# Kernel optimization log

Hardware: AMD Instinct MI355X
Metric: run time of the kernel (lower is better)

Reference implementation:

```python
import jax, jax.numpy as jnp
import numpy as np

N = 50000
E = 500000
IN_F = 128
HEADS = 4
NEG_SLOPE = 0.2


def _gatv2_conv(x, src, dst, Wl, Wr, att, bias, concat):
    # PyG GATv2Conv (share_weights=False): x_l = lin_l(x) for source, x_r = lin_r(x) for target
    n = x.shape[0]
    H, C = att.shape
    xl = (x @ Wl.T).reshape(n, H, C)
    xr = (x @ Wr.T).reshape(n, H, C)
    # per-edge: e_ij = att . leaky_relu(xl[j] + xr[i])
    e = jax.nn.leaky_relu(xl[src] + xr[dst], negative_slope=NEG_SLOPE)  # [E,H,C]
    logit = jnp.einsum('ehc,hc->eh', e, att)  # [E,H]
    # segment softmax over destination node
    lmax = jax.ops.segment_max(logit, dst, num_segments=n)
    lmax = jnp.where(jnp.isfinite(lmax), lmax, 0.0)
    w = jnp.exp(logit - lmax[dst])
    denom = jax.ops.segment_sum(w, dst, num_segments=n)
    alpha = w / (denom[dst] + 1e-16)
    # weighted scatter-aggregate of source messages
    out = jax.ops.segment_sum(xl[src] * alpha[:, :, None], dst, num_segments=n)  # [N,H,C]
    if concat:
        return out.reshape(n, H * C) + bias
    return out.mean(axis=1) + bias


def setup_inputs() -> dict:
    key = jax.random.key(0)
    ks = jax.random.split(key, 11)
    s = 0.1
    x = jax.random.normal(ks[0], (N, IN_F), jnp.float32)
    edge_index = jax.random.randint(ks[1], (2, E), 0, N, dtype=jnp.int32)
    # layer 1: in=128 -> heads=4, C=32, concat -> out 128
    Wl1 = jax.random.normal(ks[2], (128, IN_F), jnp.float32) * s
    Wr1 = jax.random.normal(ks[3], (128, IN_F), jnp.float32) * s
    att1 = jax.random.normal(ks[4], (HEADS, 32), jnp.float32) * s
    b1 = jnp.zeros((128,), jnp.float32)
    # layer 2: in=128 -> heads=4, C=64, mean (concat=False) -> out 64
    Wl2 = jax.random.normal(ks[5], (256, 128), jnp.float32) * s
    Wr2 = jax.random.normal(ks[6], (256, 128), jnp.float32) * s
    att2 = jax.random.normal(ks[7], (HEADS, 64), jnp.float32) * s
    b2 = jnp.zeros((64,), jnp.float32)
    return {"x": x, "edge_index": edge_index, "Wl1": Wl1, "Wr1": Wr1, "att1": att1,
            "b1": b1, "Wl2": Wl2, "Wr2": Wr2, "att2": att2, "b2": b2}


def reference(x, edge_index, Wl1, Wr1, att1, b1, Wl2, Wr2, att2, b2):
    n = x.shape[0]
    loops = jnp.arange(n, dtype=edge_index.dtype)
    src = jnp.concatenate([edge_index[0], loops])  # PyG add_self_loops=True
    dst = jnp.concatenate([edge_index[1], loops])
    # dropout inactive (inference); forward body: elu between layers
    h = jax.nn.elu(_gatv2_conv(x, src, dst, Wl1, Wr1, att1, b1, concat=True))
    logits = _gatv2_conv(h, src, dst, Wl2, Wr2, att2, b2, concat=False)
    return logits
```

## Files before the change

### kernel.cpp

```cpp
#include <hip/hip_runtime.h>
#include <hip/hip_bf16.h>
#include <math.h>


typedef _Float16 half2v __attribute__((ext_vector_type(2)));
typedef _Float16 half4v __attribute__((ext_vector_type(4)));
typedef _Float16 half8v __attribute__((ext_vector_type(8)));
typedef float float4v __attribute__((ext_vector_type(4)));

template <int CTRL>
static __device__ __forceinline__ float dppadd(float x) {
  int y = __builtin_amdgcn_update_dpp(0, __float_as_int(x), CTRL, 0xf, 0xf, true);
  return x + __int_as_float(y);
}

static __device__ __forceinline__ float red8dpp(float p) {
  p = dppadd<0xB1>(p);
  p = dppadd<0x4E>(p);
  p = dppadd<0x141>(p);
  return p;
}


__global__ void fused_cvt_count_kernel(
    const float* __restrict__ x,
    const float* __restrict__ wl1, const float* __restrict__ wr1,
    const float* __restrict__ wl2, const float* __restrict__ wr2,
    _Float16* __restrict__ xb, _Float16* __restrict__ wb,
    const int* __restrict__ dst, int* __restrict__ deg, int n4x, int E) {
  int i = blockIdx.x * blockDim.x + threadIdx.x;
  int stride = gridDim.x * blockDim.x;
  int total = n4x + 24576 + E;
  for (; i < total; i += stride) {
    if (i < n4x) {
      float4 v = ((const float4*)x)[i];
      half4v o = {(_Float16)v.x, (_Float16)v.y, (_Float16)v.z, (_Float16)v.w};
      ((half4v*)xb)[i] = o;
    } else if (i < n4x + 24576) {
      int fj = (i - n4x) * 4;
      const float* src;
      int so;
      if (fj < 16384) { src = wl1; so = fj; }
      else if (fj < 32768) { src = wr1; so = fj - 16384; }
      else if (fj < 65536) { src = wl2; so = fj - 32768; }
      else { src = wr2; so = fj - 65536; }
      float4 v = *(const float4*)(src + so);
      half4v o = {(_Float16)v.x, (_Float16)v.y, (_Float16)v.z, (_Float16)v.w};
      *(half4v*)(wb + fj) = o;
    } else {
      atomicAdd(&deg[dst[i - n4x - 24576]], 1);
    }
  }
}


__global__ void partial_kernel(const int* __restrict__ deg, int* __restrict__ partial, int N) {
  int t = threadIdx.x;
  int i = blockIdx.x * 256 + t;
  int v = (i < N) ? deg[i] : 0;
  v += __shfl_xor(v, 1); v += __shfl_xor(v, 2); v += __shfl_xor(v, 4);
  v += __shfl_xor(v, 8); v += __shfl_xor(v, 16); v += __shfl_xor(v, 32);
  __shared__ int ws[4];
  if ((t & 63) == 0) ws[t >> 6] = v;
  __syncthreads();
  if (t == 0) partial[blockIdx.x] = ws[0] + ws[1] + ws[2] + ws[3];
}

__global__ void scan_final_kernel(const int* __restrict__ deg, const int* __restrict__ partial,
                                  int* __restrict__ row_ptr, int* __restrict__ cursor,
                                  int N, int E, int nb) {
  __shared__ int sp[256];
  __shared__ int s[256];
  int t = threadIdx.x;
  int pv = (t < nb) ? partial[t] : 0;
  sp[t] = pv;
  __syncthreads();
  for (int off = 1; off < 256; off <<= 1) {
    int u = (t >= off) ? sp[t - off] : 0;
    __syncthreads();
    sp[t] += u;
    __syncthreads();
  }
  int blockpre = (blockIdx.x > 0) ? sp[blockIdx.x - 1] : 0;
  int i = blockIdx.x * 256 + t;
  int v = (i < N) ? deg[i] : 0;
  s[t] = v;
  __syncthreads();
  for (int off = 1; off < 256; off <<= 1) {
    int u = (t >= off) ? s[t - off] : 0;
    __syncthreads();
    s[t] += u;
    __syncthreads();
  }
  int excl = s[t] - v + blockpre;
  if (i < N) {
    row_ptr[i] = excl;
    cursor[i] = excl;
  }
  if (blockIdx.x == 0 && t == 0) row_ptr[N] = E;
}

__global__ void fill_kernel(const int* __restrict__ src, const int* __restrict__ dst,
                            int* __restrict__ cursor, int* __restrict__ col, int E) {
  int i = blockIdx.x * blockDim.x + threadIdx.x;
  if (i < E) {
    int d = dst[i];
    int pos = atomicAdd(&cursor[d], 1);
    col[pos] = src[i];
  }
}

__global__ __launch_bounds__(256) void gemm_mfma2(
    const _Float16* __restrict__ A, const _Float16* __restrict__ Wa,
    const _Float16* __restrict__ Wb, _Float16* __restrict__ Ca,
    _Float16* __restrict__ Cb, int N, int Oa, int ldC) {
  __shared__ _Float16 lds[32768];
  int t = threadIdx.x;
  int gbase = blockIdx.y * 256;
#pragma unroll
  for (int i = 0; i < 16; ++i) {
    int c = t + i * 256;
    int row = c >> 4, kc = c & 15;
    int grow = gbase + row;
    const _Float16* srcW =
        (grow < Oa) ? (Wa + (size_t)grow * 128) : (Wb + (size_t)(grow - Oa) * 128);
    half8v v = *(const half8v*)(srcW + kc * 8);
    int off16 = (row << 4) | (kc ^ (row & 7));
    *(half8v*)((char*)lds + (off16 << 4)) = v;
  }
  __syncthreads();
  int wv = t >> 6, lane = t & 63;
  int l15 = lane & 15, l4 = lane >> 4;
  int row0 = blockIdx.x * 64 + (wv & 1) * 32;
  int colw = (wv >> 1) * 128;
  int gc = gbase + colw;
  half8v xf[2][4];
#pragma unroll
  for (int rg = 0; rg < 2; ++rg) {
    int r = row0 + rg * 16 + l15;
    bool valid = r < N;
    const half8v* Ar = (const half8v*)(A + (size_t)r * 128 + l4 * 8);
#pragma unroll
    for (int kk = 0; kk < 4; ++kk) {
      half8v z = {};
      xf[rg][kk] = valid ? Ar[kk * 4] : z;
    }
  }
  int wrow = colw + l15;
  float4v acc[2][8] = {};
#pragma unroll
  for (int kk = 0; kk < 4; ++kk) {
    int xorterm = ((kk * 4 + l4) ^ (l15 & 7)) << 4;
    const char* base = (const char*)lds + wrow * 256 + xorterm;
    half8v wf[8];
#pragma unroll
    for (int ot = 0; ot < 8; ++ot) wf[ot] = *(const half8v*)(base + ot * 4096);
#pragma unroll
    for (int ot = 0; ot < 8; ++ot) {
      acc[0][ot] = __builtin_amdgcn_mfma_f32_16x16x32_f16(wf[ot], xf[0][kk], acc[0][ot], 0, 0, 0);
      acc[1][ot] = __builtin_amdgcn_mfma_f32_16x16x32_f16(wf[ot], xf[1][kk], acc[1][ot], 0, 0, 0);
    }
  }
  bool isA = gc < Oa;
  _Float16* C = isA ? Ca : Cb;
  int cb = isA ? gc : gc - Oa;
#pragma unroll
  for (int rg = 0; rg < 2; ++rg) {
    int r = row0 + rg * 16 + l15;
    if (r < N) {
#pragma unroll
      for (int ot = 0; ot < 8; ++ot) {
        half4v o = {(_Float16)acc[rg][ot][0], (_Float16)acc[rg][ot][1],
                    (_Float16)acc[rg][ot][2], (_Float16)acc[rg][ot][3]};
        *(half4v*)(C + (size_t)r * ldC + cb + ot * 16 + l4 * 4) = o;
      }
    }
  }
}


__global__ __launch_bounds__(128) void agg1_kernel(
    const _Float16* __restrict__ xl, const _Float16* __restrict__ xr,
    const float* __restrict__ att, const float* __restrict__ bias,
    const int* __restrict__ row_ptr, const int* __restrict__ col,
    _Float16* __restrict__ hout, int N) {
  int wid = (blockIdx.x * blockDim.x + threadIdx.x) >> 6;
  int lane = threadIdx.x & 63;
  if (wid >= N) return;
  int eslot = lane >> 5, sub = lane & 31;
  const uint d0 = (uint)sub * 4u;
  const float L2E = 1.44269504f;
  half4v xrv = *(const half4v*)(xr + (((uint)wid << 7) | d0));
  float4 atf = *(const float4*)(att + d0);
  half2v atlo = {(_Float16)(atf.x * L2E), (_Float16)(atf.y * L2E)};
  half2v athi = {(_Float16)(atf.z * L2E), (_Float16)(atf.w * L2E)};
  half4v k4 = {(_Float16)0.2f, (_Float16)0.2f, (_Float16)0.2f, (_Float16)0.2f};
  int e0 = row_ptr[wid];
  int deg = row_ptr[wid + 1] - e0;
  const int* ecol = col + e0;
  float s, a0, a1, a2, a3;
  {
    half4v v = *(const half4v*)(xl + (((uint)wid << 7) | d0));
    half4v u = v + xrv;
    half4v lr = __builtin_elementwise_max(u, u * k4);
    float p = __builtin_amdgcn_fdot2((half2v){lr.x, lr.y}, atlo, 0.f, false);
    p = __builtin_amdgcn_fdot2((half2v){lr.z, lr.w}, athi, p, false);
    p = red8dpp(p);
    float w = (eslot == 0) ? exp2f(p) : 0.f;
    s = w;
    a0 = w * (float)v.x; a1 = w * (float)v.y; a2 = w * (float)v.z; a3 = w * (float)v.w;
  }
  if (deg > 0) {
    int dm1 = deg - 1;
    int idx = eslot;
    int cA = ecol[min(idx, dm1)];
    int cB = ecol[min(idx + 2, dm1)];
    half4v vA = *(const half4v*)(xl + (((uint)cA << 7) | d0));
    half4v vB = *(const half4v*)(xl + (((uint)cB << 7) | d0));
    int M = deg >> 1;
    for (int j = 0; j < M; ++j) {
      int cC = ecol[min(idx + 4, dm1)];
      half4v vC = *(const half4v*)(xl + (((uint)cC << 7) | d0));
      half4v u = vA + xrv;
      half4v lr = __builtin_elementwise_max(u, u * k4);
      float p = __builtin_amdgcn_fdot2((half2v){lr.x, lr.y}, atlo, 0.f, false);
      p = __builtin_amdgcn_fdot2((half2v){lr.z, lr.w}, athi, p, false);
      p = red8dpp(p);
      float w = exp2f(p);
      s += w;
      a0 = fmaf(w, (float)vA.x, a0);
      a1 = fmaf(w, (float)vA.y, a1);
      a2 = fmaf(w, (float)vA.z, a2);
      a3 = fmaf(w, (float)vA.w, a3);
      vA = vB; vB = vC; idx += 2;
    }
    if (deg & 1) {
      half4v u = vA + xrv;
      half4v lr = __builtin_elementwise_max(u, u * k4);
      float p = __builtin_amdgcn_fdot2((half2v){lr.x, lr.y}, atlo, 0.f, false);
      p = __builtin_amdgcn_fdot2((half2v){lr.z, lr.w}, athi, p, false);
      p = red8dpp(p);
      float w = (eslot == 0) ? exp2f(p) : 0.f;
      s += w;
      a0 = fmaf(w, (float)vA.x, a0);
      a1 = fmaf(w, (float)vA.y, a1);
      a2 = fmaf(w, (float)vA.z, a2);
      a3 = fmaf(w, (float)vA.w, a3);
    }
  }
  s += __shfl_xor(s, 32);
  a0 += __shfl_xor(a0, 32); a1 += __shfl_xor(a1, 32);
  a2 += __shfl_xor(a2, 32); a3 += __shfl_xor(a3, 32);
  float inv = 1.f / (s + 1e-16f);
  float4 bi = *(const float4*)(bias + d0);
  float o0 = a0 * inv + bi.x, o1 = a1 * inv + bi.y;
  float o2 = a2 * inv + bi.z, o3 = a3 * inv + bi.w;
  o0 = o0 > 0.f ? o0 : __expf(o0) - 1.f;
  o1 = o1 > 0.f ? o1 : __expf(o1) - 1.f;
  o2 = o2 > 0.f ? o2 : __expf(o2) - 1.f;
  o3 = o3 > 0.f ? o3 : __expf(o3) - 1.f;
  if (eslot == 0) {
    half4v o = {(_Float16)o0, (_Float16)o1, (_Float16)o2, (_Float16)o3};
    *(half4v*)(hout + (((uint)wid << 7) | d0)) = o;
  }
}

__global__ __launch_bounds__(128) void agg2_kernel(
    const _Float16* __restrict__ xl, const _Float16* __restrict__ xr,
    const float* __restrict__ att, const float* __restrict__ bias,
    const int* __restrict__ row_ptr, const int* __restrict__ col,
    float* __restrict__ out, int N) {
  int wid = (blockIdx.x * blockDim.x + threadIdx.x) >> 6;
  int lane = threadIdx.x & 63;
  if (wid >= N) return;
  int eslot = lane >> 5, sub = lane & 31;
  const uint d0 = (uint)sub * 8u;
  const float L2E = 1.44269504f;
  half8v xrv = *(const half8v*)(xr + (((uint)wid << 8) | d0));
  float4 af0 = *(const float4*)(att + d0);
  float4 af1 = *(const float4*)(att + d0 + 4);
  half2v at[4] = {{(_Float16)(af0.x * L2E), (_Float16)(af0.y * L2E)},
                  {(_Float16)(af0.z * L2E), (_Float16)(af0.w * L2E)},
                  {(_Float16)(af1.x * L2E), (_Float16)(af1.y * L2E)},
                  {(_Float16)(af1.z * L2E), (_Float16)(af1.w * L2E)}};
  half8v k8 = {(_Float16)0.2f, (_Float16)0.2f, (_Float16)0.2f, (_Float16)0.2f,
               (_Float16)0.2f, (_Float16)0.2f, (_Float16)0.2f, (_Float16)0.2f};
  int e0 = row_ptr[wid];
  int deg = row_ptr[wid + 1] - e0;
  const int* ecol = col + e0;
  float s, ac[8];
  {
    half8v v = *(const half8v*)(xl + (((uint)wid << 8) | d0));
    half8v u = v + xrv;
    half8v lr = __builtin_elementwise_max(u, u * k8);
    float p = __builtin_amdgcn_fdot2((half2v){lr[0], lr[1]}, at[0], 0.f, false);
    p = __builtin_amdgcn_fdot2((half2v){lr[2], lr[3]}, at[1], p, false);
    p = __builtin_amdgcn_fdot2((half2v){lr[4], lr[5]}, at[2], p, false);
    p = __builtin_amdgcn_fdot2((half2v){lr[6], lr[7]}, at[3], p, false);
    p = red8dpp(p);
    float w = (eslot == 0) ? exp2f(p) : 0.f;
    s = w;
#pragma unroll
    for (int k = 0; k < 8; ++k) ac[k] = w * (float)v[k];
  }
  if (deg > 0) {
    int dm1 = deg - 1;
    int idx = eslot;
    int cA = ecol[min(idx, dm1)];
    int cB = ecol[min(idx + 2, dm1)];
    half8v vA = *(const half8v*)(xl + (((uint)cA << 8) | d0));
    half8v vB = *(const half8v*)(xl + (((uint)cB << 8) | d0));
    int M = deg >> 1;
    for (int j = 0; j < M; ++j) {
      int cC = ecol[min(idx + 4, dm1)];
      half8v vC = *(const half8v*)(xl + (((uint)cC << 8) | d0));
      half8v u = vA + xrv;
      half8v lr = __builtin_elementwise_max(u, u * k8);
      float p = __builtin_amdgcn_fdot2((half2v){lr[0], lr[1]}, at[0], 0.f, false);
      p = __builtin_amdgcn_fdot2((half2v){lr[2], lr[3]}, at[1], p, false);
      p = __builtin_amdgcn_fdot2((half2v){lr[4], lr[5]}, at[2], p, false);
      p = __builtin_amdgcn_fdot2((half2v){lr[6], lr[7]}, at[3], p, false);
      p = red8dpp(p);
      float w = exp2f(p);
      s += w;
#pragma unroll
      for (int k = 0; k < 8; ++k) ac[k] = fmaf(w, (float)vA[k], ac[k]);
      vA = vB; vB = vC; idx += 2;
    }
    if (deg & 1) {
      half8v u = vA + xrv;
      half8v lr = __builtin_elementwise_max(u, u * k8);
      float p = __builtin_amdgcn_fdot2((half2v){lr[0], lr[1]}, at[0], 0.f, false);
      p = __builtin_amdgcn_fdot2((half2v){lr[2], lr[3]}, at[1], p, false);
      p = __builtin_amdgcn_fdot2((half2v){lr[4], lr[5]}, at[2], p, false);
      p = __builtin_amdgcn_fdot2((half2v){lr[6], lr[7]}, at[3], p, false);
      p = red8dpp(p);
      float w = (eslot == 0) ? exp2f(p) : 0.f;
      s += w;
#pragma unroll
      for (int k = 0; k < 8; ++k) ac[k] = fmaf(w, (float)vA[k], ac[k]);
    }
  }
  s += __shfl_xor(s, 32);
#pragma unroll
  for (int k = 0; k < 8; ++k) ac[k] += __shfl_xor(ac[k], 32);
  float inv = 1.f / (s + 1e-16f);
#pragma unroll
  for (int k = 0; k < 8; ++k) ac[k] *= inv;
#pragma unroll
  for (int k = 0; k < 8; ++k) {
    ac[k] += __shfl_xor(ac[k], 8);
    ac[k] += __shfl_xor(ac[k], 16);
  }
  if (lane < 8) {
    float4 b0 = *(const float4*)(bias + lane * 8);
    float4 b1v = *(const float4*)(bias + lane * 8 + 4);
    float4 o0 = make_float4(ac[0] * 0.25f + b0.x, ac[1] * 0.25f + b0.y,
                            ac[2] * 0.25f + b0.z, ac[3] * 0.25f + b0.w);
    float4 o1 = make_float4(ac[4] * 0.25f + b1v.x, ac[5] * 0.25f + b1v.y,
                            ac[6] * 0.25f + b1v.z, ac[7] * 0.25f + b1v.w);
    float* op = out + (size_t)wid * 64 + lane * 8;
    *(float4*)op = o0;
    *(float4*)(op + 4) = o1;
  }
}

extern "C" void kernel_launch(void* const* d_in, const int* in_sizes, int n_in,
                              void* d_out, int out_size, void* d_ws, size_t ws_size,
                              hipStream_t stream) {
  const float* x = (const float*)d_in[0];
  const int* ei = (const int*)d_in[1];
  const float* Wl1 = (const float*)d_in[2];
  const float* Wr1 = (const float*)d_in[3];
  const float* att1 = (const float*)d_in[4];
  const float* b1 = (const float*)d_in[5];
  const float* Wl2 = (const float*)d_in[6];
  const float* Wr2 = (const float*)d_in[7];
  const float* att2 = (const float*)d_in[8];
  const float* b2 = (const float*)d_in[9];
  float* out = (float*)d_out;

  int N = in_sizes[0] / 128;
  int E = in_sizes[1] / 2;
  const int* srcArr = ei;
  const int* dstArr = ei + E;

  char* w = (char*)d_ws;
  auto alloc = [&](size_t bytes) {
    char* p = w;
    w += (bytes + 255) & ~(size_t)255;
    return p;
  };
  int* row_ptr = (int*)alloc((size_t)(N + 1) * sizeof(int));
  int* cursor = (int*)alloc((size_t)N * sizeof(int));
  int* partial = (int*)alloc(256 * sizeof(int));
  int* col = (int*)alloc((size_t)E * sizeof(int));
  _Float16* xb = (_Float16*)alloc((size_t)N * 128 * 2);
  _Float16* wb = (_Float16*)alloc(98304 * 2);
  _Float16* hb = (_Float16*)alloc((size_t)N * 128 * 2);
  _Float16* xl1 = (_Float16*)alloc((size_t)N * 128 * 2);
  _Float16* xr1 = (_Float16*)alloc((size_t)N * 128 * 2);
  _Float16* xl2 = (_Float16*)alloc((size_t)N * 256 * 2);
  _Float16* xr2 = (_Float16*)alloc((size_t)N * 256 * 2);

  const _Float16* wl1b = wb;
  const _Float16* wr1b = wb + 16384;
  const _Float16* wl2b = wb + 32768;
  const _Float16* wr2b = wb + 65536;

  hipMemsetAsync(cursor, 0, (size_t)N * sizeof(int), stream);
  fused_cvt_count_kernel<<<2048, 256, 0, stream>>>(x, Wl1, Wr1, Wl2, Wr2, xb, wb,
                                                   dstArr, cursor, N * 32, E);

  int nb = (N + 255) / 256;
  partial_kernel<<<nb, 256, 0, stream>>>(cursor, partial, N);
  scan_final_kernel<<<nb, 256, 0, stream>>>(cursor, partial, row_ptr, cursor, N, E, nb);
  fill_kernel<<<(E + 255) / 256, 256, 0, stream>>>(srcArr, dstArr, cursor, col, E);

  int gx = (N + 63) / 64;
  int aggBlocks = (N * 64 + 127) / 128;
  gemm_mfma2<<<dim3(gx, 1), 256, 0, stream>>>(xb, wl1b, wr1b, xl1, xr1, N, 128, 128);
  agg1_kernel<<<aggBlocks, 128, 0, stream>>>(xl1, xr1, att1, b1, row_ptr, col, hb, N);

  gemm_mfma2<<<dim3(gx, 2), 256, 0, stream>>>(hb, wl2b, wr2b, xl2, xr2, N, 256, 256);
  agg2_kernel<<<aggBlocks, 128, 0, stream>>>(xl2, xr2, att2, b2, row_ptr, col, out, N);
}
```

Baseline: 190.7 us.

## Deepen gather prefetch and accumulate layer-2 aggregation in fp16

Both aggregation kernels now keep three neighbour rows in flight instead of two, and their loops are unrolled by three, so more gather latency is hidden. The layer-2 kernel also accumulates the weighted messages in packed fp16 rather than eight fp32 FMAs. It subtracts a fixed shift of 10 from the logit before the exponent so fp16 is less likely to overflow. This cuts ALU work and registers, but fp16 accumulation loses precision and can still overflow or underflow for logits far from the shift.

```diff
diff --git a/kernel.cpp b/kernel.cpp
--- a/kernel.cpp
+++ b/kernel.cpp
@@ -212,15 +212,18 @@
   }
   if (deg > 0) {
     int dm1 = deg - 1;
-    int idx = eslot;
-    int cA = ecol[min(idx, dm1)];
-    int cB = ecol[min(idx + 2, dm1)];
+    int cA = ecol[min(eslot, dm1)];
+    int cB = ecol[min(eslot + 2, dm1)];
+    int cC = ecol[min(eslot + 4, dm1)];
     half4v vA = *(const half4v*)(xl + (((uint)cA << 7) | d0));
     half4v vB = *(const half4v*)(xl + (((uint)cB << 7) | d0));
+    half4v vC = *(const half4v*)(xl + (((uint)cC << 7) | d0));
     int M = deg >> 1;
+    int pf = eslot + 6;
+#pragma unroll 3
     for (int j = 0; j < M; ++j) {
-      int cC = ecol[min(idx + 4, dm1)];
-      half4v vC = *(const half4v*)(xl + (((uint)cC << 7) | d0));
+      int cD = ecol[min(pf, dm1)];
+      half4v vD = *(const half4v*)(xl + (((uint)cD << 7) | d0));
       half4v u = vA + xrv;
       half4v lr = __builtin_elementwise_max(u, u * k4);
       float p = __builtin_amdgcn_fdot2((half2v){lr.x, lr.y}, atlo, 0.f, false);
@@ -232,7 +235,7 @@
       a1 = fmaf(w, (float)vA.y, a1);
       a2 = fmaf(w, (float)vA.z, a2);
       a3 = fmaf(w, (float)vA.w, a3);
-      vA = vB; vB = vC; idx += 2;
+      vA = vB; vB = vC; vC = vD; pf += 2;
     }
     if (deg & 1) {
       half4v u = vA + xrv;
@@ -276,6 +279,7 @@
   int eslot = lane >> 5, sub = lane & 31;
   const uint d0 = (uint)sub * 8u;
   const float L2E = 1.44269504f;
+  const float SH = 10.f;
   half8v xrv = *(const half8v*)(xr + (((uint)wid << 8) | d0));
   float4 af0 = *(const float4*)(att + d0);
   float4 af1 = *(const float4*)(att + d0 + 4);
@@ -288,7 +292,8 @@
   int e0 = row_ptr[wid];
   int deg = row_ptr[wid + 1] - e0;
   const int* ecol = col + e0;
-  float s, ac[8];
+  float s;
+  half8v ach;
   {
     half8v v = *(const half8v*)(xl + (((uint)wid << 8) | d0));
     half8v u = v + xrv;
@@ -298,22 +303,26 @@
     p = __builtin_amdgcn_fdot2((half2v){lr[4], lr[5]}, at[2], p, false);
     p = __builtin_amdgcn_fdot2((half2v){lr[6], lr[7]}, at[3], p, false);
     p = red8dpp(p);
-    float w = (eslot == 0) ? exp2f(p) : 0.f;
+    float w = (eslot == 0) ? exp2f(p - SH) : 0.f;
     s = w;
-#pragma unroll
-    for (int k = 0; k < 8; ++k) ac[k] = w * (float)v[k];
+    _Float16 wh = (_Float16)w;
+    half8v w8 = {wh, wh, wh, wh, wh, wh, wh, wh};
+    ach = v * w8;
   }
   if (deg > 0) {
     int dm1 = deg - 1;
-    int idx = eslot;
-    int cA = ecol[min(idx, dm1)];
-    int cB = ecol[min(idx + 2, dm1)];
+    int cA = ecol[min(eslot, dm1)];
+    int cB = ecol[min(eslot + 2, dm1)];
+    int cC = ecol[min(eslot + 4, dm1)];
     half8v vA = *(const half8v*)(xl + (((uint)cA << 8) | d0));
     half8v vB = *(const half8v*)(xl + (((uint)cB << 8) | d0));
+    half8v vC = *(const half8v*)(xl + (((uint)cC << 8) | d0));
     int M = deg >> 1;
+    int pf = eslot + 6;
+#pragma unroll 3
     for (int j = 0; j < M; ++j) {
-      int cC = ecol[min(idx + 4, dm1)];
-      half8v vC = *(const half8v*)(xl + (((uint)cC << 8) | d0));
+      int cD = ecol[min(pf, dm1)];
+      half8v vD = *(const half8v*)(xl + (((uint)cD << 8) | d0));
       half8v u = vA + xrv;
       half8v lr = __builtin_elementwise_max(u, u * k8);
       float p = __builtin_amdgcn_fdot2((half2v){lr[0], lr[1]}, at[0], 0.f, false);
@@ -321,11 +330,12 @@
       p = __builtin_amdgcn_fdot2((half2v){lr[4], lr[5]}, at[2], p, false);
       p = __builtin_amdgcn_fdot2((half2v){lr[6], lr[7]}, at[3], p, false);
       p = red8dpp(p);
-      float w = exp2f(p);
+      float w = exp2f(p - SH);
       s += w;
-#pragma unroll
-      for (int k = 0; k < 8; ++k) ac[k] = fmaf(w, (float)vA[k], ac[k]);
-      vA = vB; vB = vC; idx += 2;
+      _Float16 wh = (_Float16)w;
+      half8v w8 = {wh, wh, wh, wh, wh, wh, wh, wh};
+      ach += vA * w8;
+      vA = vB; vB = vC; vC = vD; pf += 2;
     }
     if (deg & 1) {
       half8v u = vA + xrv;
@@ -335,15 +345,20 @@
       p = __builtin_amdgcn_fdot2((half2v){lr[4], lr[5]}, at[2], p, false);
       p = __builtin_amdgcn_fdot2((half2v){lr[6], lr[7]}, at[3], p, false);
       p = red8dpp(p);
-      float w = (eslot == 0) ? exp2f(p) : 0.f;
+      float w = (eslot == 0) ? exp2f(p - SH) : 0.f;
       s += w;
-#pragma unroll
-      for (int k = 0; k < 8; ++k) ac[k] = fmaf(w, (float)vA[k], ac[k]);
+      _Float16 wh = (_Float16)w;
+      half8v w8 = {wh, wh, wh, wh, wh, wh, wh, wh};
+      ach += vA * w8;
     }
   }
   s += __shfl_xor(s, 32);
-#pragma unroll
-  for (int k = 0; k < 8; ++k) ac[k] += __shfl_xor(ac[k], 32);
+  float ac[8];
+#pragma unroll
+  for (int k = 0; k < 8; ++k) {
+    ac[k] = (float)ach[k];
+    ac[k] += __shfl_xor(ac[k], 32);
+  }
   float inv = 1.f / (s + 1e-16f);
 #pragma unroll
   for (int k = 0; k < 8; ++k) ac[k] *= inv;
```

Measured after the change: 190.9 us. About the same (+0.1%).

## Process four edges per wave with wider per-lane feature vectors in GAT aggregation

Applied to the files above, without the earlier changes.

Both aggregation kernels now split the 64-lane wave into four edge slots of 16 lanes instead of two slots of 32. Each lane handles twice as many features (8 halves in layer 1, 16 in layer 2), so per-head dot-product reductions need one fewer DPP step. The loop keeps a three-deep prefetch of neighbour rows and is partially unrolled, aiming for more gathers in flight per wave and fewer loop iterations. In exchange, each lane holds more registers for accumulators and prefetch buffers, and the final cross-slot reduction needs extra shuffles, which may lower occupancy.

```diff
diff --git a/kernel.cpp b/kernel.cpp
--- a/kernel.cpp
+++ b/kernel.cpp
@@ -14,10 +14,9 @@
   return x + __int_as_float(y);
 }
 
-static __device__ __forceinline__ float red8dpp(float p) {
+static __device__ __forceinline__ float red4dpp(float p) {
   p = dppadd<0xB1>(p);
   p = dppadd<0x4E>(p);
-  p = dppadd<0x141>(p);
   return p;
 }
 
@@ -187,81 +186,71 @@
   int wid = (blockIdx.x * blockDim.x + threadIdx.x) >> 6;
   int lane = threadIdx.x & 63;
   if (wid >= N) return;
-  int eslot = lane >> 5, sub = lane & 31;
-  const uint d0 = (uint)sub * 4u;
+  int eslot = lane >> 4, sub = lane & 15;
+  const uint d0 = (uint)sub * 8u;
   const float L2E = 1.44269504f;
-  half4v xrv = *(const half4v*)(xr + (((uint)wid << 7) | d0));
-  float4 atf = *(const float4*)(att + d0);
-  half2v atlo = {(_Float16)(atf.x * L2E), (_Float16)(atf.y * L2E)};
-  half2v athi = {(_Float16)(atf.z * L2E), (_Float16)(atf.w * L2E)};
-  half4v k4 = {(_Float16)0.2f, (_Float16)0.2f, (_Float16)0.2f, (_Float16)0.2f};
+  half8v xrv = *(const half8v*)(xr + (((uint)wid << 7) | d0));
+  float4 af0 = *(const float4*)(att + d0);
+  float4 af1 = *(const float4*)(att + d0 + 4);
+  half2v at4[4] = {{(_Float16)(af0.x * L2E), (_Float16)(af0.y * L2E)},
+                   {(_Float16)(af0.z * L2E), (_Float16)(af0.w * L2E)},
+                   {(_Float16)(af1.x * L2E), (_Float16)(af1.y * L2E)},
+                   {(_Float16)(af1.z * L2E), (_Float16)(af1.w * L2E)}};
+  half8v k8 = {(_Float16)0.2f, (_Float16)0.2f, (_Float16)0.2f, (_Float16)0.2f,
+               (_Float16)0.2f, (_Float16)0.2f, (_Float16)0.2f, (_Float16)0.2f};
   int e0 = row_ptr[wid];
   int deg = row_ptr[wid + 1] - e0;
   const int* ecol = col + e0;
-  float s, a0, a1, a2, a3;
-  {
-    half4v v = *(const half4v*)(xl + (((uint)wid << 7) | d0));
-    half4v u = v + xrv;
-    half4v lr = __builtin_elementwise_max(u, u * k4);
-    float p = __builtin_amdgcn_fdot2((half2v){lr.x, lr.y}, atlo, 0.f, false);
-    p = __builtin_amdgcn_fdot2((half2v){lr.z, lr.w}, athi, p, false);
-    p = red8dpp(p);
-    float w = (eslot == 0) ? exp2f(p) : 0.f;
-    s = w;
-    a0 = w * (float)v.x; a1 = w * (float)v.y; a2 = w * (float)v.z; a3 = w * (float)v.w;
-  }
+  float s = 0.f, a[8] = {};
+  auto edge = [&](half8v v, bool valid) {
+    half8v u = v + xrv;
+    half8v lr = __builtin_elementwise_max(u, u * k8);
+    float pA = __builtin_amdgcn_fdot2((half2v){lr[0], lr[1]}, at4[0], 0.f, false);
+    pA = __builtin_amdgcn_fdot2((half2v){lr[2], lr[3]}, at4[1], pA, false);
+    float pB = __builtin_amdgcn_fdot2((half2v){lr[4], lr[5]}, at4[2], 0.f, false);
+    pB = __builtin_amdgcn_fdot2((half2v){lr[6], lr[7]}, at4[3], pB, false);
+    float p = red4dpp(pA + pB);
+    float w = valid ? exp2f(p) : 0.f;
+    s += w;
+#pragma unroll
+    for (int k = 0; k < 8; ++k) a[k] = fmaf(w, (float)v[k], a[k]);
+  };
+  auto ld = [&](uint node) { return *(const half8v*)(xl + ((node << 7) | d0)); };
+  edge(ld((uint)wid), eslot == 0);
   if (deg > 0) {
     int dm1 = deg - 1;
-    int idx = eslot;
-    int cA = ecol[min(idx, dm1)];
-    int cB = ecol[min(idx + 2, dm1)];
-    half4v vA = *(const half4v*)(xl + (((uint)cA << 7) | d0));
-    half4v vB = *(const half4v*)(xl + (((uint)cB << 7) | d0));
-    int M = deg >> 1;
+    half8v vA = ld((uint)ecol[min(eslot, dm1)]);
+    half8v vB = ld((uint)ecol[min(eslot + 4, dm1)]);
+    half8v vC = ld((uint)ecol[min(eslot + 8, dm1)]);
+    int M = deg >> 2, pf = eslot + 12;
+#pragma unroll 2
     for (int j = 0; j < M; ++j) {
-      int cC = ecol[min(idx + 4, dm1)];
-      half4v vC = *(const half4v*)(xl + (((uint)cC << 7) | d0));
-      half4v u = vA + xrv;
-      half4v lr = __builtin_elementwise_max(u, u * k4);
-      float p = __builtin_amdgcn_fdot2((half2v){lr.x, lr.y}, atlo, 0.f, false);
-      p = __builtin_amdgcn_fdot2((half2v){lr.z, lr.w}, athi, p, false);
-      p = red8dpp(p);
-      float w = exp2f(p);
-      s += w;
-      a0 = fmaf(w, (float)vA.x, a0);
-      a1 = fmaf(w, (float)vA.y, a1);
-      a2 = fmaf(w, (float)vA.z, a2);
-      a3 = fmaf(w, (float)vA.w, a3);
-      vA = vB; vB = vC; idx += 2;
-    }
-    if (deg & 1) {
-      half4v u = vA + xrv;
-      half4v lr = __builtin_elementwise_max(u, u * k4);
-      float p = __builtin_amdgcn_fdot2((half2v){lr.x, lr.y}, atlo, 0.f, false);
-      p = __builtin_amdgcn_fdot2((half2v){lr.z, lr.w}, athi, p, false);
-      p = red8dpp(p);
-      float w = (eslot == 0) ? exp2f(p) : 0.f;
-      s += w;
-      a0 = fmaf(w, (float)vA.x, a0);
-      a1 = fmaf(w, (float)vA.y, a1);
-      a2 = fmaf(w, (float)vA.z, a2);
-      a3 = fmaf(w, (float)vA.w, a3);
-    }
-  }
-  s += __shfl_xor(s, 32);
-  a0 += __shfl_xor(a0, 32); a1 += __shfl_xor(a1, 32);
-  a2 += __shfl_xor(a2, 32); a3 += __shfl_xor(a3, 32);
+      half8v vD = ld((uint)ecol[min(pf, dm1)]);
+      edge(vA, true);
+      vA = vB; vB = vC; vC = vD; pf += 4;
+    }
+    int T = deg & 3;
+    if (T) edge(vA, eslot < T);
+  }
+  s += __shfl_xor(s, 16); s += __shfl_xor(s, 32);
+#pragma unroll
+  for (int k = 0; k < 8; ++k) {
+    a[k] += __shfl_xor(a[k], 16);
+    a[k] += __shfl_xor(a[k], 32);
+  }
   float inv = 1.f / (s + 1e-16f);
-  float4 bi = *(const float4*)(bias + d0);
-  float o0 = a0 * inv + bi.x, o1 = a1 * inv + bi.y;
-  float o2 = a2 * inv + bi.z, o3 = a3 * inv + bi.w;
-  o0 = o0 > 0.f ? o0 : __expf(o0) - 1.f;
-  o1 = o1 > 0.f ? o1 : __expf(o1) - 1.f;
-  o2 = o2 > 0.f ? o2 : __expf(o2) - 1.f;
-  o3 = o3 > 0.f ? o3 : __expf(o3) - 1.f;
   if (eslot == 0) {
-    half4v o = {(_Float16)o0, (_Float16)o1, (_Float16)o2, (_Float16)o3};
-    *(half4v*)(hout + (((uint)wid << 7) | d0)) = o;
+    float4 b0 = *(const float4*)(bias + d0);
+    float4 b1 = *(const float4*)(bias + d0 + 4);
+    float bb[8] = {b0.x, b0.y, b0.z, b0.w, b1.x, b1.y, b1.z, b1.w};
+    half8v o;
+#pragma unroll
+    for (int k = 0; k < 8; ++k) {
+      float tv = a[k] * inv + bb[k];
+      tv = tv > 0.f ? tv : __expf(tv) - 1.f;
+      o[k] = (_Float16)tv;
+    }
+    *(half8v*)(hout + (((uint)wid << 7) | d0)) = o;
   }
 }
 
@@ -273,95 +262,96 @@
   int wid = (blockIdx.x * blockDim.x + threadIdx.x) >> 6;
   int lane = threadIdx.x & 63;
   if (wid >= N) return;
-  int eslot = lane >> 5, sub = lane & 31;
-  const uint d0 = (uint)sub * 8u;
+  int eslot = lane >> 4, sub = lane & 15;
+  const uint d0 = (uint)sub * 16u;
   const float L2E = 1.44269504f;
-  half8v xrv = *(const half8v*)(xr + (((uint)wid << 8) | d0));
-  float4 af0 = *(const float4*)(att + d0);
-  float4 af1 = *(const float4*)(att + d0 + 4);
-  half2v at[4] = {{(_Float16)(af0.x * L2E), (_Float16)(af0.y * L2E)},
-                  {(_Float16)(af0.z * L2E), (_Float16)(af0.w * L2E)},
-                  {(_Float16)(af1.x * L2E), (_Float16)(af1.y * L2E)},
-                  {(_Float16)(af1.z * L2E), (_Float16)(af1.w * L2E)}};
+  const _Float16* xrp = xr + (((uint)wid << 8) | d0);
+  half8v xra = *(const half8v*)xrp;
+  half8v xrb = *(const half8v*)(xrp + 8);
+  half2v at8[8];
+#pragma unroll
+  for (int k = 0; k < 8; ++k) {
+    float2 af = *(const float2*)(att + d0 + 2 * k);
+    at8[k] = {(_Float16)(af.x * L2E), (_Float16)(af.y * L2E)};
+  }
   half8v k8 = {(_Float16)0.2f, (_Float16)0.2f, (_Float16)0.2f, (_Float16)0.2f,
                (_Float16)0.2f, (_Float16)0.2f, (_Float16)0.2f, (_Float16)0.2f};
   int e0 = row_ptr[wid];
   int deg = row_ptr[wid + 1] - e0;
   const int* ecol = col + e0;
-  float s, ac[8];
+  float s = 0.f, a[16] = {};
+  auto edge = [&](half8v va, half8v vb, bool valid) {
+    half8v ua = va + xra;
+    half8v ub = vb + xrb;
+    half8v la = __builtin_elementwise_max(ua, ua * k8);
+    half8v lb = __builtin_elementwise_max(ub, ub * k8);
+    float pA = __builtin_amdgcn_fdot2((half2v){la[0], la[1]}, at8[0], 0.f, false);
+    pA = __builtin_amdgcn_fdot2((half2v){la[2], la[3]}, at8[1], pA, false);
+    pA = __builtin_amdgcn_fdot2((half2v){la[4], la[5]}, at8[2], pA, false);
+    pA = __builtin_amdgcn_fdot2((half2v){la[6], la[7]}, at8[3], pA, false);
+    float pB = __builtin_amdgcn_fdot2((half2v){lb[0], lb[1]}, at8[4], 0.f, false);
+    pB = __builtin_amdgcn_fdot2((half2v){lb[2], lb[3]}, at8[5], pB, false);
+    pB = __builtin_amdgcn_fdot2((half2v){lb[4], lb[5]}, at8[6], pB, false);
+    pB = __builtin_amdgcn_fdot2((half2v){lb[6], lb[7]}, at8[7], pB, false);
+    float p = red4dpp(pA + pB);
+    float w = valid ? exp2f(p) : 0.f;
+    s += w;
+#pragma unroll
+    for (int k = 0; k < 8; ++k) a[k] = fmaf(w, (float)va[k], a[k]);
+#pragma unroll
+    for (int k = 0; k < 8; ++k) a[8 + k] = fmaf(w, (float)vb[k], a[8 + k]);
+  };
+  auto ld = [&](uint node, half8v& va, half8v& vb) {
+    const _Float16* p = xl + ((node << 8) | d0);
+    va = *(const half8v*)p;
+    vb = *(const half8v*)(p + 8);
+  };
   {
-    half8v v = *(const half8v*)(xl + (((uint)wid << 8) | d0));
-    half8v u = v + xrv;
-    half8v lr = __builtin_elementwise_max(u, u * k8);
-    float p = __builtin_amdgcn_fdot2((half2v){lr[0], lr[1]}, at[0], 0.f, false);
-    p = __builtin_amdgcn_fdot2((half2v){lr[2], lr[3]}, at[1], p, false);
-    p = __builtin_amdgcn_fdot2((half2v){lr[4], lr[5]}, at[2], p, false);
-    p = __builtin_amdgcn_fdot2((half2v){lr[6], lr[7]}, at[3], p, false);
-    p = red8dpp(p);
-    float w = (eslot == 0) ? exp2f(p) : 0.f;
-    s = w;
-#pragma unroll
-    for (int k = 0; k < 8; ++k) ac[k] = w * (float)v[k];
+    half8v sva, svb;
+    ld((uint)wid, sva, svb);
+    edge(sva, svb, eslot == 0);
   }
   if (deg > 0) {
     int dm1 = deg - 1;
-    int idx = eslot;
-    int cA = ecol[min(idx, dm1)];
-    int cB = ecol[min(idx + 2, dm1)];
-    half8v vA = *(const half8v*)(xl + (((uint)cA << 8) | d0));
-    half8v vB = *(const half8v*)(xl + (((uint)cB << 8) | d0));
-    int M = deg >> 1;
+    half8v vA0, vA1, vB0, vB1, vC0, vC1;
+    ld((uint)ecol[min(eslot, dm1)], vA0, vA1);
+    ld((uint)ecol[min(eslot + 4, dm1)], vB0, vB1);
+    ld((uint)ecol[min(eslot + 8, dm1)], vC0, vC1);
+    int M = deg >> 2, pf = eslot + 12;
+#pragma unroll 2
     for (int j = 0; j < M; ++j) {
-      int cC = ecol[min(idx + 4, dm1)];
-      half8v vC = *(const half8v*)(xl + (((uint)cC << 8) | d0));
-      half8v u = vA + xrv;
-      half8v lr = __builtin_elementwise_max(u, u * k8);
-      float p = __builtin_amdgcn_fdot2((half2v){lr[0], lr[1]}, at[0], 0.f, false);
-      p = __builtin_amdgcn_fdot2((half2v){lr[2], lr[3]}, at[1], p, false);
-      p = __builtin_amdgcn_fdot2((half2v){lr[4], lr[5]}, at[2], p, false);
-      p = __builtin_amdgcn_fdot2((half2v){lr[6], lr[7]}, at[3], p, false);
-      p = red8dpp(p);
-      float w = exp2f(p);
-      s += w;
-#pragma unroll
-      for (int k = 0; k < 8; ++k) ac[k] = fmaf(w, (float)vA[k], ac[k]);
-      vA = vB; vB = vC; idx += 2;
-    }
-    if (deg & 1) {
-      half8v u = vA + xrv;
-      half8v lr = __builtin_elementwise_max(u, u * k8);
-      float p = __builtin_amdgcn_fdot2((half2v){lr[0], lr[1]}, at[0], 0.f, false);
-      p = __builtin_amdgcn_fdot2((half2v){lr[2], lr[3]}, at[1], p, false);
-      p = __builtin_amdgcn_fdot2((half2v){lr[4], lr[5]}, at[2], p, false);
-      p = __builtin_amdgcn_fdot2((half2v){lr[6], lr[7]}, at[3], p, false);
-      p = red8dpp(p);
-      float w = (eslot == 0) ? exp2f(p) : 0.f;
-      s += w;
-#pragma unroll
-      for (int k = 0; k < 8; ++k) ac[k] = fmaf(w, (float)vA[k], ac[k]);
-    }
-  }
-  s += __shfl_xor(s, 32);
-#pragma unroll
-  for (int k = 0; k < 8; ++k) ac[k] += __shfl_xor(ac[k], 32);
+      half8v vD0, vD1;
+      ld((uint)ecol[min(pf, dm1)], vD0, vD1);
+      edge(vA0, vA1, true);
+      vA0 = vB0; vA1 = vB1; vB0 = vC0; vB1 = vC1; vC0 = vD0; vC1 = vD1;
+      pf += 4;
+    }
+    int T = deg & 3;
+    if (T) edge(vA0, vA1, eslot < T);
+  }
+  s += __shfl_xor(s, 16); s += __shfl_xor(s, 32);
+#pragma unroll
+  for (int k = 0; k < 16; ++k) {
+    a[k] += __shfl_xor(a[k], 16);
+    a[k] += __shfl_xor(a[k], 32);
+  }
   float inv = 1.f / (s + 1e-16f);
 #pragma unroll
-  for (int k = 0; k < 8; ++k) ac[k] *= inv;
-#pragma unroll
-  for (int k = 0; k < 8; ++k) {
-    ac[k] += __shfl_xor(ac[k], 8);
-    ac[k] += __shfl_xor(ac[k], 16);
-  }
-  if (lane < 8) {
-    float4 b0 = *(const float4*)(bias + lane * 8);
-    float4 b1v = *(const float4*)(bias + lane * 8 + 4);
-    float4 o0 = make_float4(ac[0] * 0.25f + b0.x, ac[1] * 0.25f + b0.y,
-                            ac[2] * 0.25f + b0.z, ac[3] * 0.25f + b0.w);
-    float4 o1 = make_float4(ac[4] * 0.25f + b1v.x, ac[5] * 0.25f + b1v.y,
-                            ac[6] * 0.25f + b1v.z, ac[7] * 0.25f + b1v.w);
-    float* op = out + (size_t)wid * 64 + lane * 8;
-    *(float4*)op = o0;
-    *(float4*)(op + 4) = o1;
+  for (int k = 0; k < 16; ++k) a[k] *= inv;
+#pragma unroll
+  for (int k = 0; k < 16; ++k) {
+    a[k] += __shfl_xor(a[k], 4);
+    a[k] += __shfl_xor(a[k], 8);
+  }
+  if (lane < 4) {
+    float* op = out + (size_t)wid * 64 + lane * 16;
+#pragma unroll
+    for (int q = 0; q < 4; ++q) {
+      float4 b = *(const float4*)(bias + lane * 16 + q * 4);
+      float4 o = make_float4(a[q * 4 + 0] * 0.25f + b.x, a[q * 4 + 1] * 0.25f + b.y,
+                             a[q * 4 + 2] * 0.25f + b.z, a[q * 4 + 3] * 0.25f + b.w);
+      *(float4*)(op + q * 4) = o;
+    }
   }
 }
 
```

New measurement: 196.4 us. 3.0% more time.
